# Optimization experiments

Hardware: AMD Instinct MI355X
Metric: run time of the kernel (lower is better)

Reference implementation:

```python
import jax, jax.numpy as jnp
import numpy as np
from jax import lax

K = 8
SCALE = 100.0

# ---- straight-through binarizers (match torch custom Functions) ----
@jax.custom_vjp
def bin_w(x):
    return jnp.sign(x)

def _bin_w_fwd(x):
    return jnp.sign(x), None

def _bin_w_bwd(_, g):
    return (g,)  # identity STE

bin_w.defvjp(_bin_w_fwd, _bin_w_bwd)

@jax.custom_vjp
def bin_a(x):
    return jnp.sign(x)

def _bin_a_fwd(x):
    return jnp.sign(x), x

def _bin_a_bwd(x, g):
    return (g * jnp.clip(2.0 - jnp.abs(2.0 * x), 0.0, None),)

bin_a.defvjp(_bin_a_fwd, _bin_a_bwd)

# ---- SDP sampling with custom backward (grad_z scaled by sqrt(scale)) ----
@jax.custom_vjp
def sdp(m, z, rv):
    # m: (N,), z: (K,N), rv: (1,K) -> w: (N,)
    return (rv @ z)[0] + m

def _sdp_fwd(m, z, rv):
    return (rv @ z)[0] + m, rv

def _sdp_bwd(rv, g):
    grad_m = g
    grad_z = (rv.T @ g[None, :]) * np.sqrt(SCALE)  # (K,N)
    return (grad_m, grad_z, jnp.zeros_like(rv))

sdp.defvjp(_sdp_fwd, _sdp_bwd)

def _forward(x, M, Z, alpha, rv):
    N = M.size
    m = M.reshape(N)          # (N,)
    z = Z.reshape(K, N)       # (K,N)
    # no_grad normalization of m,z data: value changes, gradient passes through identity
    A = m * m + jnp.sum(z * z, axis=0) / SCALE
    inv = lax.rsqrt(A)
    m_used = m + lax.stop_gradient(m * inv - m)
    z_used = z + lax.stop_gradient(z * inv - z)
    w = sdp(m_used, z_used, rv)               # (N,)
    bw = bin_w(w).reshape(M.shape)            # (O,I,3,3) in {-1,+1}
    ba = bin_a(x)                             # (B,C,H,W) in {-1,+1}
    out = lax.conv_general_dilated(
        ba, bw, window_strides=(1, 1), padding=((1, 1), (1, 1)),
        dimension_numbers=('NCHW', 'OIHW', 'NCHW'))
    return out * alpha  # alpha (O,1,1) broadcasts over (B,O,H,W)

def setup_inputs() -> dict:
    key = jax.random.key(0)
    k1, k2, k3, k4, k5 = jax.random.split(key, 5)
    x = jax.random.normal(k1, (64, 256, 28, 28), dtype=jnp.float32)
    M = jax.random.normal(k2, (256, 256, 3, 3), dtype=jnp.float32)
    Z = jax.random.normal(k3, (8, 256, 256, 3, 3), dtype=jnp.float32)
    alpha = jax.random.uniform(k4, (256, 1, 1), dtype=jnp.float32)
    rv = jax.random.normal(k5, (1, 8), dtype=jnp.float32) * np.float32(1.0 / np.sqrt(SCALE))
    return {"x": x, "M": M, "Z": Z, "alpha": alpha, "rv": rv}

def reference(x, M, Z, alpha, rv):
    return _forward(x, M, Z, alpha, rv)
```

## Files before the change

### kernel.cpp

```cpp
#include <hip/hip_runtime.h>
#include <stdint.h>

typedef unsigned int uint32;

#define BB 64
#define CC 256
#define OO 256
#define HH 28
#define WW 28
#define HWP 784
#define NWT 589824

__global__ __launch_bounds__(256) void pack_x_kernel(
    const float* __restrict__ x, uint32* __restrict__ apack) {
  int p = blockIdx.x * 256 + threadIdx.x;
  int j = blockIdx.y;
  int b = blockIdx.z;
  if (p >= HWP) return;
  const float* xp = x + ((size_t)(b * CC + j * 32) * HWP) + p;
  uint32 m = 0;
#pragma unroll
  for (int cc = 0; cc < 32; ++cc) {
    float v = xp[(size_t)cc * HWP];
    m |= ((uint32)(v > 0.0f)) << cc;
  }
  apack[((size_t)b * HWP + p) * 8 + j] = m;
}

__global__ __launch_bounds__(256) void pack_w_kernel(
    const float* __restrict__ M, const float* __restrict__ Z,
    const float* __restrict__ rv, uint32* __restrict__ wpack) {
  __shared__ float sacc[576];
  const int o = blockIdx.x;
  const int jh = blockIdx.y;
  const int tid = threadIdx.x;
  const size_t base = (size_t)o * 2304 + (size_t)jh * 576;

  float r[8];
#pragma unroll
  for (int k = 0; k < 8; ++k) r[k] = rv[k];

#pragma unroll
  for (int ii = 0; ii < 3; ++ii) {
    int i = tid + ii * 256;
    if (i < 576) {
      float s = M[base + i];
#pragma unroll
      for (int k = 0; k < 8; ++k) s += r[k] * Z[(size_t)k * NWT + base + i];
      sacc[i] = s;
    }
  }
  __syncthreads();

  if (tid < 18) {
    int tap = tid % 9;
    int jj = tid / 9;
    uint32 m = 0;
#pragma unroll
    for (int cc = 0; cc < 32; ++cc) {
      float v = sacc[(jj * 32 + cc) * 9 + tap];
      m |= ((uint32)(v > 0.0f)) << cc;
    }
    wpack[(o * 9 + tap) * 8 + jh * 2 + jj] = m;
  }
}

__global__ __launch_bounds__(256) void ptab_kernel(
    const uint32* __restrict__ wpack, const float* __restrict__ alpha,
    float* __restrict__ ptabA, uint32* __restrict__ ptabP) {
  int o = threadIdx.x;
  const uint32* wt = wpack + (size_t)o * 72;
  int pt[9];
#pragma unroll
  for (int t = 0; t < 9; ++t) {
    int s = 0;
#pragma unroll
    for (int j = 0; j < 8; ++j) s += __popc(wt[t * 8 + j]);
    pt[t] = s;
  }
  int row0 = pt[0] + pt[1] + pt[2], row2 = pt[6] + pt[7] + pt[8];
  int col0 = pt[0] + pt[3] + pt[6], col2 = pt[2] + pt[5] + pt[8];
  float a = alpha[o];
  const int nv[9] = {4, 6, 4, 6, 9, 6, 4, 6, 4};
  int S[9];
  S[0] = row0 + col0 - pt[0]; S[1] = row0; S[2] = row0 + col2 - pt[2];
  S[3] = col0;                S[4] = 0;    S[5] = col2;
  S[6] = row2 + col0 - pt[6]; S[7] = row2; S[8] = row2 + col2 - pt[8];
#pragma unroll
  for (int c = 0; c < 9; ++c)
    ptabA[o * 9 + c] = a * (float)(256 * nv[c] + 2 * S[c]);
  ptabP[o * 4 + 0] = __float_as_uint(-2.0f * a);
  ptabP[o * 4 + 1] = (uint32)col0;
  ptabP[o * 4 + 2] = (uint32)col2;
  ptabP[o * 4 + 3] = 0;
}

#define BCNT_ACC(T, x) asm("v_bcnt_u32_b32 %0, %1, %0" : "+v"(T) : "v"(x))

__global__ __launch_bounds__(256, 8) void conv_kernel(
    const uint32* __restrict__ apack, const uint32* __restrict__ wpack,
    const float* __restrict__ ptabA, const uint32* __restrict__ ptabP,
    float* __restrict__ out) {
  __shared__ float atab[16 * 9];

  const int rg = blockIdx.x;
  const int og = blockIdx.y;
  const int b  = blockIdx.z;
  const int tid = threadIdx.x;
  const int lane = tid & 63;
  const int wv = tid >> 6;
  const int w = lane & 31;
  const int rb = rg * 16 + wv * 4 + (lane >> 5) * 2;
  const bool wact = w < WW;

  if (tid < 144) atab[tid] = ptabA[og * 144 + tid];
  __syncthreads();

  const int wcl = wact ? w : (WW - 1);
  uint4 A[4][2];
#pragma unroll
  for (int i = 0; i < 4; ++i) {
    int rr = rb - 1 + i;
    bool v = (rr >= 0) && (rr < HH);
    const uint4* src =
        (const uint4*)(apack + ((size_t)(b * HWP + (v ? rr : 0) * WW + wcl)) * 8);
    uint4 lo = src[0], hi = src[1];
    if (!v) { lo = make_uint4(0, 0, 0, 0); hi = make_uint4(0, 0, 0, 0); }
    A[i][0] = lo;
    A[i][1] = hi;
  }

  const int wc = (w == 0) ? 0 : (w == WW - 1 ? 2 : 1);
  const int r1v = rb + 1;
  const int hc0 = (rb == 0) ? 0 : (rb == HH - 1 ? 2 : 1);
  const int hc1 = (r1v == 0) ? 0 : (r1v == HH - 1 ? 2 : 1);
  const int cls0 = hc0 * 3 + wc;
  const int cls1 = hc1 * 3 + wc;

  const size_t obase = ((size_t)b * OO + og * 16) * HWP + (size_t)rb * WW + w;
  const bool st0 = wact && (rb < HH);
  const bool st1 = wact && (r1v < HH);

  for (int oi = 0; oi < 16; ++oi) {
    const int o = og * 16 + oi;
    const int wo = __builtin_amdgcn_readfirstlane(o * 72);
    const uint32* wt = wpack + wo;
    const uint4 pm = ((const uint4*)ptabP)[o];
    const float m = __uint_as_float(pm.x);

    uint32 T00 = 0, T01 = 0, T02 = 0, T10 = 0, T11 = 0, T12 = 0;
#pragma unroll
    for (int dh = 0; dh < 3; ++dh) {
      const uint32* a0 = (const uint32*)&A[dh][0];
      const uint32* a1 = (const uint32*)&A[dh + 1][0];
#pragma unroll
      for (int j = 0; j < 8; ++j) {
        const uint32 w0 = wt[(dh * 3 + 0) * 8 + j];
        const uint32 w1 = wt[(dh * 3 + 1) * 8 + j];
        const uint32 w2 = wt[(dh * 3 + 2) * 8 + j];
        const uint32 av0 = a0[j], av1 = a1[j];
        BCNT_ACC(T00, av0 ^ w0);
        BCNT_ACC(T01, av0 ^ w1);
        BCNT_ACC(T02, av0 ^ w2);
        BCNT_ACC(T10, av1 ^ w0);
        BCNT_ACC(T11, av1 ^ w1);
        BCNT_ACC(T12, av1 ^ w2);
      }
    }
    uint32 pl = __shfl_up(T00 | (T10 << 16), 1);
    uint32 pr = __shfl_down(T02 | (T12 << 16), 1);
    if (w == 0)      pl = pm.y * 0x10001u;
    if (w == WW - 1) pr = pm.z * 0x10001u;
    uint32 tp = pl + (T01 | (T11 << 16)) + pr;
    float r0 = fmaf(m, (float)(tp & 0xffffu), atab[oi * 9 + cls0]);
    float r1 = fmaf(m, (float)(tp >> 16), atab[oi * 9 + cls1]);
    if (st0) out[obase + (size_t)oi * HWP] = r0;
    if (st1) out[obase + (size_t)oi * HWP + WW] = r1;
  }
}

extern "C" void kernel_launch(void* const* d_in, const int* in_sizes, int n_in,
                              void* d_out, int out_size, void* d_ws,
                              size_t ws_size, hipStream_t stream) {
  const float* x     = (const float*)d_in[0];
  const float* M     = (const float*)d_in[1];
  const float* Z     = (const float*)d_in[2];
  const float* alpha = (const float*)d_in[3];
  const float* rv    = (const float*)d_in[4];
  float* out = (float*)d_out;

  uint32* apack = (uint32*)d_ws;
  uint32* wpack = (uint32*)((char*)d_ws + 1605632);
  float*  ptabA = (float*)((char*)d_ws + 1679360);
  uint32* ptabP = (uint32*)((char*)d_ws + 1688576);

  pack_x_kernel<<<dim3(4, 8, BB), 256, 0, stream>>>(x, apack);
  pack_w_kernel<<<dim3(256, 4), 256, 0, stream>>>(M, Z, rv, wpack);
  ptab_kernel<<<dim3(1), 256, 0, stream>>>(wpack, alpha, ptabA, ptabP);
  conv_kernel<<<dim3(2, 16, BB), 256, 0, stream>>>(apack, wpack, ptabA, ptabP,
                                                   out);
}
```

Before: 192.0 us.

## Fuse ptab computation into weight packing and pin activation registers in conv

Merges the single-block ptab kernel into pack_w_kernel so each block handles a full output channel, computes all 72 packed words, and derives the per-channel correction table in shared memory. This removes one launch and a serialized single-block kernel, at the cost of a grid of 256 blocks instead of 1024 for the weight packing. The conv kernel's launch bound drops from 8 to 4 blocks per SM, giving the compiler more registers. Empty asm barriers force the loaded activation words to stay in VGPRs rather than be rematerialized or reloaded.

```diff
diff --git a/kernel.cpp b/kernel.cpp
--- a/kernel.cpp
+++ b/kernel.cpp
@@ -29,75 +29,73 @@
 
 __global__ __launch_bounds__(256) void pack_w_kernel(
     const float* __restrict__ M, const float* __restrict__ Z,
-    const float* __restrict__ rv, uint32* __restrict__ wpack) {
-  __shared__ float sacc[576];
+    const float* __restrict__ rv, const float* __restrict__ alpha,
+    uint32* __restrict__ wpack, float* __restrict__ ptabA,
+    uint32* __restrict__ ptabP) {
+  __shared__ float sacc[2304];
+  __shared__ uint32 ww[72];
   const int o = blockIdx.x;
-  const int jh = blockIdx.y;
   const int tid = threadIdx.x;
-  const size_t base = (size_t)o * 2304 + (size_t)jh * 576;
+  const size_t base = (size_t)o * 2304;
 
   float r[8];
 #pragma unroll
   for (int k = 0; k < 8; ++k) r[k] = rv[k];
 
 #pragma unroll
-  for (int ii = 0; ii < 3; ++ii) {
+  for (int ii = 0; ii < 9; ++ii) {
     int i = tid + ii * 256;
-    if (i < 576) {
-      float s = M[base + i];
-#pragma unroll
-      for (int k = 0; k < 8; ++k) s += r[k] * Z[(size_t)k * NWT + base + i];
-      sacc[i] = s;
-    }
+    float s = M[base + i];
+#pragma unroll
+    for (int k = 0; k < 8; ++k) s += r[k] * Z[(size_t)k * NWT + base + i];
+    sacc[i] = s;
   }
   __syncthreads();
 
-  if (tid < 18) {
+  if (tid < 72) {
     int tap = tid % 9;
-    int jj = tid / 9;
+    int j = tid / 9;
     uint32 m = 0;
 #pragma unroll
     for (int cc = 0; cc < 32; ++cc) {
-      float v = sacc[(jj * 32 + cc) * 9 + tap];
+      float v = sacc[(j * 32 + cc) * 9 + tap];
       m |= ((uint32)(v > 0.0f)) << cc;
     }
-    wpack[(o * 9 + tap) * 8 + jh * 2 + jj] = m;
-  }
-}
-
-__global__ __launch_bounds__(256) void ptab_kernel(
-    const uint32* __restrict__ wpack, const float* __restrict__ alpha,
-    float* __restrict__ ptabA, uint32* __restrict__ ptabP) {
-  int o = threadIdx.x;
-  const uint32* wt = wpack + (size_t)o * 72;
-  int pt[9];
-#pragma unroll
-  for (int t = 0; t < 9; ++t) {
-    int s = 0;
-#pragma unroll
-    for (int j = 0; j < 8; ++j) s += __popc(wt[t * 8 + j]);
-    pt[t] = s;
-  }
-  int row0 = pt[0] + pt[1] + pt[2], row2 = pt[6] + pt[7] + pt[8];
-  int col0 = pt[0] + pt[3] + pt[6], col2 = pt[2] + pt[5] + pt[8];
-  float a = alpha[o];
-  const int nv[9] = {4, 6, 4, 6, 9, 6, 4, 6, 4};
-  int S[9];
-  S[0] = row0 + col0 - pt[0]; S[1] = row0; S[2] = row0 + col2 - pt[2];
-  S[3] = col0;                S[4] = 0;    S[5] = col2;
-  S[6] = row2 + col0 - pt[6]; S[7] = row2; S[8] = row2 + col2 - pt[8];
-#pragma unroll
-  for (int c = 0; c < 9; ++c)
-    ptabA[o * 9 + c] = a * (float)(256 * nv[c] + 2 * S[c]);
-  ptabP[o * 4 + 0] = __float_as_uint(-2.0f * a);
-  ptabP[o * 4 + 1] = (uint32)col0;
-  ptabP[o * 4 + 2] = (uint32)col2;
-  ptabP[o * 4 + 3] = 0;
+    ww[tap * 8 + j] = m;
+    wpack[(size_t)o * 72 + tap * 8 + j] = m;
+  }
+  __syncthreads();
+
+  if (tid == 0) {
+    int pt[9];
+#pragma unroll
+    for (int t = 0; t < 9; ++t) {
+      int s = 0;
+#pragma unroll
+      for (int j = 0; j < 8; ++j) s += __popc(ww[t * 8 + j]);
+      pt[t] = s;
+    }
+    int row0 = pt[0] + pt[1] + pt[2], row2 = pt[6] + pt[7] + pt[8];
+    int col0 = pt[0] + pt[3] + pt[6], col2 = pt[2] + pt[5] + pt[8];
+    float a = alpha[o];
+    const int nv[9] = {4, 6, 4, 6, 9, 6, 4, 6, 4};
+    int S[9];
+    S[0] = row0 + col0 - pt[0]; S[1] = row0; S[2] = row0 + col2 - pt[2];
+    S[3] = col0;                S[4] = 0;    S[5] = col2;
+    S[6] = row2 + col0 - pt[6]; S[7] = row2; S[8] = row2 + col2 - pt[8];
+#pragma unroll
+    for (int c = 0; c < 9; ++c)
+      ptabA[o * 9 + c] = a * (float)(256 * nv[c] + 2 * S[c]);
+    ptabP[o * 4 + 0] = __float_as_uint(-2.0f * a);
+    ptabP[o * 4 + 1] = (uint32)col0;
+    ptabP[o * 4 + 2] = (uint32)col2;
+    ptabP[o * 4 + 3] = 0;
+  }
 }
 
 #define BCNT_ACC(T, x) asm("v_bcnt_u32_b32 %0, %1, %0" : "+v"(T) : "v"(x))
 
-__global__ __launch_bounds__(256, 8) void conv_kernel(
+__global__ __launch_bounds__(256, 4) void conv_kernel(
     const uint32* __restrict__ apack, const uint32* __restrict__ wpack,
     const float* __restrict__ ptabA, const uint32* __restrict__ ptabP,
     float* __restrict__ out) {
@@ -128,6 +126,13 @@
     if (!v) { lo = make_uint4(0, 0, 0, 0); hi = make_uint4(0, 0, 0, 0); }
     A[i][0] = lo;
     A[i][1] = hi;
+  }
+  {
+    uint32* aw = (uint32*)A;
+#pragma unroll
+    for (int i = 0; i < 32; i += 4)
+      asm volatile("" : "+v"(aw[i]), "+v"(aw[i + 1]), "+v"(aw[i + 2]),
+                        "+v"(aw[i + 3]));
   }
 
   const int wc = (w == 0) ? 0 : (w == WW - 1 ? 2 : 1);
@@ -195,8 +200,8 @@
   uint32* ptabP = (uint32*)((char*)d_ws + 1688576);
 
   pack_x_kernel<<<dim3(4, 8, BB), 256, 0, stream>>>(x, apack);
-  pack_w_kernel<<<dim3(256, 4), 256, 0, stream>>>(M, Z, rv, wpack);
-  ptab_kernel<<<dim3(1), 256, 0, stream>>>(wpack, alpha, ptabA, ptabP);
+  pack_w_kernel<<<dim3(256), 256, 0, stream>>>(M, Z, rv, alpha, wpack, ptabA,
+                                               ptabP);
   conv_kernel<<<dim3(2, 16, BB), 256, 0, stream>>>(apack, wpack, ptabA, ptabP,
                                                    out);
 }
```

New measurement: 187.6 us. 2.3% less time.
